# Kernel tuning notes

Measured on AMD Instinct MI355X. Metric: run time of the kernel, lower is better.

## Reference

```python
import jax, jax.numpy as jnp
import numpy as np

B, L, D = 8, 2048, 256
D_MODEL = 1024
NUM_SIGNALS = 16
MAX_POSITIONS = 4096
ROLE_OUTPUT = 2  # role id used for the CLS token


def setup_inputs() -> dict:
    key = jax.random.key(0)
    ks = jax.random.split(key, 12)
    emb = jax.random.normal(ks[0], (B, L, D), dtype=jnp.float32)
    pos = jax.random.randint(ks[1], (B, L), 1, MAX_POSITIONS + 1)          # pos >= 1 for real tokens
    sid = jax.random.randint(ks[2], (B, L), 0, NUM_SIGNALS)
    role = jax.random.randint(ks[3], (B, L), 0, 3)
    padding_mask = jax.random.uniform(ks[4], (B, L)) < 0.75                # True = real token
    # learned parameters
    proj_W = jax.random.normal(ks[5], (NUM_SIGNALS, D_MODEL, D), dtype=jnp.float32) * (1.0 / np.sqrt(D))
    proj_b = jax.random.normal(ks[6], (NUM_SIGNALS, D_MODEL), dtype=jnp.float32) * 0.01
    cls_content = jax.random.normal(ks[7], (D_MODEL,), dtype=jnp.float32)
    pos_embed = jax.random.normal(ks[8], (MAX_POSITIONS + 1, D_MODEL), dtype=jnp.float32)
    id_embed = jax.random.normal(ks[9], (NUM_SIGNALS + 1, D_MODEL), dtype=jnp.float32)
    role_embed = jax.random.normal(ks[10], (3, D_MODEL), dtype=jnp.float32)
    return dict(emb=emb, pos=pos, sid=sid, role=role, padding_mask=padding_mask,
                proj_W=proj_W, proj_b=proj_b, cls_content=cls_content,
                pos_embed=pos_embed, id_embed=id_embed, role_embed=role_embed)


def reference(emb, pos, sid, role, padding_mask,
              proj_W, proj_b, cls_content, pos_embed, id_embed, role_embed):
    Bv, Lv, _ = emb.shape
    S, d_model, _ = proj_W.shape
    cls_id = S

    # Grouped per-signal projection: one GEMM per signal id, select per token.
    tokens = jnp.zeros((Bv, Lv, d_model), dtype=emb.dtype)
    for s in range(S):
        proj_s = jnp.einsum('bld,ed->ble', emb, proj_W[s]) + proj_b[s]   # (B, L, d_model)
        keep = ((sid == s) & padding_mask)[..., None]
        tokens = jnp.where(keep, proj_s, tokens)

    # Prepend CLS
    cls = jnp.broadcast_to(cls_content[None, None, :], (Bv, 1, d_model))
    tokens = jnp.concatenate([cls, tokens], axis=1)                       # (B, L+1, d_model)

    pos_full = jnp.concatenate([jnp.zeros((Bv, 1), dtype=pos.dtype), pos], axis=1)
    sid_full = jnp.concatenate([jnp.full((Bv, 1), cls_id, dtype=sid.dtype), sid], axis=1)
    role_full = jnp.concatenate([jnp.full((Bv, 1), ROLE_OUTPUT, dtype=role.dtype), role], axis=1)

    tokens = tokens + pos_embed[pos_full] + id_embed[sid_full] + role_embed[role_full]

    attn_keep = jnp.concatenate([jnp.ones((Bv, 1), dtype=bool), padding_mask], axis=1)
    return tokens, attn_keep
```

## Files before the change

kernel.cpp:

```cpp
#include <hip/hip_runtime.h>
#include <hip/hip_bf16.h>
#include <stdint.h>

#define B_ 8
#define L_ 2048
#define NTOK 16384
#define DK 256
#define DM 1024
#define NS 16
#define LOUT 2049
#define TOK_OUT (B_*LOUT*DM)
#define ATTN_OUT (B_*LOUT)

typedef unsigned short u16;
typedef unsigned int u32;
typedef __bf16 bf16x8 __attribute__((ext_vector_type(8)));
typedef float f32x4 __attribute__((ext_vector_type(4)));

__device__ inline u32 packbf2(float lo, float hi) {
    u32 a, b;
    __builtin_memcpy(&a, &lo, 4);
    __builtin_memcpy(&b, &hi, 4);
    a = (a + 0x8000u) >> 16;
    b = (b + 0x8000u) & 0xFFFF0000u;
    return a | b;
}

__device__ inline void gll16(const void* g, void* l) {
    __builtin_amdgcn_global_load_lds(
        (const __attribute__((address_space(1))) unsigned int*)g,
        (__attribute__((address_space(3))) unsigned int*)l, 16, 0, 0);
}

#define WS_CNT 0
#define WS_CUR 16
#define WS_PERM 64
#define WS_MASK (64 + NTOK)
#define A_OFF 262144ULL
#define APAD_ROWS 18432
#define W_OFF (A_OFF + (unsigned long long)APAD_ROWS * 512ULL)
#define WS_NEED (W_OFF + 16384ULL * 512ULL)

__global__ __launch_bounds__(256) void p1_kernel(const unsigned char* __restrict__ mb,
                                                 const int* __restrict__ sid,
                                                 int* __restrict__ wsi) {
    __shared__ int f_c1ge2, f_ge2, f_odd;
    __shared__ int lcnt[NS];
    int tid = threadIdx.x;
    if (tid == 0) { f_c1ge2 = 0; f_ge2 = 0; f_odd = 0; }
    if (tid < NS) lcnt[tid] = 0;
    __syncthreads();

    int c1ge2 = 0, ge2 = 0, oddnz = 0;
    const u32* mw = (const u32*)mb;
    #pragma unroll
    for (int i = 0; i < 16; i++) {
        u32 x = mw[tid * 16 + i];
        u32 b0 = x & 0xFF, b1 = (x >> 8) & 0xFF, b2 = (x >> 16) & 0xFF, b3 = x >> 24;
        if (b1 >= 2) c1ge2 = 1;
        if (b0 >= 2 || b1 >= 2 || b2 >= 2 || b3 >= 2) ge2 = 1;
        if ((b1 | b3) != 0) oddnz = 1;
    }
    if (c1ge2) atomicOr(&f_c1ge2, 1);
    if (ge2) atomicOr(&f_ge2, 1);
    if (oddnz) atomicOr(&f_odd, 1);
    __syncthreads();

    int width;
    if (f_c1ge2) width = 2;
    else if (f_ge2) width = 4;
    else if (f_odd) width = 1;
    else width = 4;

    int t = blockIdx.x * 256 + tid;
    int m;
    if (width == 1) m = (mb[t] != 0);
    else if (width == 2) m = (((const u16*)mb)[t] != 0);
    else m = (((const u32*)mb)[t] != 0);

    wsi[WS_MASK + t] = m;
    if (m) atomicAdd(&lcnt[sid[t]], 1);
    __syncthreads();
    if (tid < NS) atomicAdd(&wsi[WS_CNT + tid], lcnt[tid]);
}

__global__ __launch_bounds__(256) void p3_kernel(const int* __restrict__ sid,
                                                 int* __restrict__ wsi) {
    __shared__ int gcnt[NS], lcnt[NS], base[NS];
    int tid = threadIdx.x;
    if (tid < NS) { gcnt[tid] = wsi[WS_CNT + tid]; lcnt[tid] = 0; }
    __syncthreads();
    int t = blockIdx.x * 256 + tid;
    int m = wsi[WS_MASK + t];
    int s = sid[t];
    int r = 0;
    if (m) r = atomicAdd(&lcnt[s], 1);
    __syncthreads();
    if (tid < NS) {
        int off = 0;
        for (int i = 0; i < tid; i++) off += gcnt[i];
        base[tid] = off + atomicAdd(&wsi[WS_CUR + tid], lcnt[tid]);
    }
    __syncthreads();
    if (m) wsi[WS_PERM + base[s] + r] = t;
}

__global__ __launch_bounds__(256) void prep_kernel(const float* __restrict__ emb,
                                                   const float* __restrict__ W,
                                                   int* __restrict__ wsi,
                                                   unsigned char* __restrict__ wsb) {
    int bid = blockIdx.x;
    int tid = threadIdx.x;
    int lane = tid & 63;
    int wv = tid >> 6;
    if (bid < 4608) {
        int cnts[NS], segoff[NS], pbase[NS];
        int accp = 0, accu = 0;
        #pragma unroll
        for (int i = 0; i < NS; i++) {
            cnts[i] = wsi[WS_CNT + i];
            segoff[i] = accp; pbase[i] = accu;
            accp += ((cnts[i] + 127) >> 7) << 7;
            accu += cnts[i];
        }
        int r = bid * 4 + wv;
        if (r >= accp) return;
        int s = 0;
        #pragma unroll
        for (int i = 1; i < NS; i++) if (r >= segoff[i]) s = i;
        int local = r - segoff[s];
        u16* Ab = (u16*)(wsb + A_OFF);
        uint2 o;
        if (local < cnts[s]) {
            int t = wsi[WS_PERM + pbase[s] + local];
            float4 a = *(const float4*)(emb + (size_t)t * DK + lane * 4);
            o.x = packbf2(a.x, a.y);
            o.y = packbf2(a.z, a.w);
        } else {
            o.x = 0; o.y = 0;
        }
        *(uint2*)(Ab + (size_t)r * DK + lane * 4) = o;
    } else {
        int r = (bid - 4608) * 4 + wv;
        u16* Wb = (u16*)(wsb + W_OFF);
        float4 a = *(const float4*)(W + (size_t)r * DK + lane * 4);
        uint2 o;
        o.x = packbf2(a.x, a.y);
        o.y = packbf2(a.z, a.w);
        *(uint2*)(Wb + (size_t)r * DK + lane * 4) = o;
    }
}

__global__ __launch_bounds__(256) void gemm_big(
    const int* __restrict__ pos, const int* __restrict__ role,
    const float* __restrict__ bias,
    const float* __restrict__ pos_emb, const float* __restrict__ id_emb,
    const float* __restrict__ role_emb,
    const int* __restrict__ wsi, const unsigned char* __restrict__ wsb,
    float* __restrict__ out) {
    __shared__ u16 As[128 * 64];
    __shared__ u16 Bs[128 * 64];
    __shared__ int toks[128];
    int tid = threadIdx.x;
    int lane = tid & 63;
    int wv = tid >> 6;

    int cnts[NS];
    #pragma unroll
    for (int i = 0; i < NS; i++) cnts[i] = wsi[WS_CNT + i];
    int ry = (int)blockIdx.y;
    int s = -1, lrt = 0, seg0 = 0, pb = 0;
    {
        int accp = 0, accu = 0;
        #pragma unroll
        for (int i = 0; i < NS; i++) {
            int rt = (cnts[i] + 127) >> 7;
            if (s < 0) {
                if (ry < rt) { s = i; lrt = ry; seg0 = accp; pb = accu; }
                else ry -= rt;
            }
            accp += rt << 7;
            accu += cnts[i];
        }
    }
    if (s < 0) return;
    int rowsValid = cnts[s] - lrt * 128;
    if (rowsValid > 128) rowsValid = 128;

    if (tid < 128) toks[tid] = (tid < rowsValid) ? wsi[WS_PERM + pb + lrt * 128 + tid] : -1;

    int n0 = (int)blockIdx.x * 128;
    const u16* Ab = (const u16*)(wsb + A_OFF) + (size_t)(seg0 + lrt * 128) * DK;
    const u16* Bb = (const u16*)(wsb + W_OFF) + (size_t)(s * DM + n0) * DK;

    int srow = lane >> 3;
    int sseg = (lane & 7) ^ srow;

    f32x4 acc[4][4];
    #pragma unroll
    for (int im = 0; im < 4; im++)
        #pragma unroll
        for (int jn = 0; jn < 4; jn++) acc[im][jn] = (f32x4){0.f, 0.f, 0.f, 0.f};

    int wm = wv >> 1, wn = wv & 1;
    int mcol = lane & 15;
    int quad = lane >> 4;

    for (int kc = 0; kc < 4; ++kc) {
        #pragma unroll
        for (int i = 0; i < 4; i++) {
            int row = wv * 32 + i * 8;
            gll16(Ab + (size_t)(row + srow) * DK + kc * 64 + sseg * 8,
                  As + row * 64);
            gll16(Bb + (size_t)(row + srow) * DK + kc * 64 + sseg * 8,
                  Bs + row * 64);
        }
        __syncthreads();
        #pragma unroll
        for (int ks = 0; ks < 2; ++ks) {
            bf16x8 af[4], bf[4];
            #pragma unroll
            for (int im = 0; im < 4; im++) {
                int row = wm * 64 + im * 16 + mcol;
                int sg = (ks * 4 + quad) ^ (row & 7);
                af[im] = *(const bf16x8*)(As + row * 64 + sg * 8);
            }
            #pragma unroll
            for (int jn = 0; jn < 4; jn++) {
                int row = wn * 64 + jn * 16 + mcol;
                int sg = (ks * 4 + quad) ^ (row & 7);
                bf[jn] = *(const bf16x8*)(Bs + row * 64 + sg * 8);
            }
            #pragma unroll
            for (int im = 0; im < 4; im++)
                #pragma unroll
                for (int jn = 0; jn < 4; jn++)
                    acc[im][jn] = __builtin_amdgcn_mfma_f32_16x16x32_bf16(
                        af[im], bf[jn], acc[im][jn], 0, 0, 0);
        }
        __syncthreads();
    }

    float bc[4];
    #pragma unroll
    for (int jn = 0; jn < 4; jn++) {
        int col = n0 + wn * 64 + jn * 16 + mcol;
        bc[jn] = bias[s * DM + col] + id_emb[s * DM + col];
    }
    #pragma unroll
    for (int im = 0; im < 4; im++) {
        #pragma unroll
        for (int r = 0; r < 4; r++) {
            int rowT = wm * 64 + im * 16 + quad * 4 + r;
            if (rowT >= rowsValid) continue;
            int t = toks[rowT];
            int p = pos[t];
            int ro = role[t];
            int b = t >> 11, l = t & 2047;
            size_t orow = (size_t)(b * LOUT + l + 1) * DM;
            #pragma unroll
            for (int jn = 0; jn < 4; jn++) {
                int col = n0 + wn * 64 + jn * 16 + mcol;
                float val = acc[im][jn][r] + bc[jn]
                    + pos_emb[(size_t)p * DM + col]
                    + role_emb[ro * DM + col];
                out[orow + col] = val;
            }
        }
    }
}

#define SP 136
__global__ __launch_bounds__(256) void gemm_small(
    const float* __restrict__ emb, const int* __restrict__ pos,
    const int* __restrict__ role,
    const float* __restrict__ W, const float* __restrict__ bias,
    const float* __restrict__ pos_emb, const float* __restrict__ id_emb,
    const float* __restrict__ role_emb,
    const int* __restrict__ wsi, float* __restrict__ out) {
    __shared__ u16 As[64 * SP];
    __shared__ u16 Bs[64 * SP];
    __shared__ int toks[64];
    int tid = threadIdx.x;

    int cnts[NS];
    #pragma unroll
    for (int i = 0; i < NS; i++) cnts[i] = wsi[WS_CNT + i];
    int ry = (int)blockIdx.y;
    int s = -1, tokOff = 0, lrt = 0;
    #pragma unroll
    for (int i = 0; i < NS; i++) {
        int rt = (cnts[i] + 63) >> 6;
        if (s < 0) {
            if (ry < rt) { s = i; lrt = ry; }
            else { ry -= rt; tokOff += cnts[i]; }
        }
    }
    if (s < 0) return;
    int idx0 = tokOff + lrt * 64;
    int v = cnts[s] - lrt * 64;
    if (v > 64) v = 64;

    if (tid < 64) toks[tid] = (tid < v) ? wsi[WS_PERM + idx0 + tid] : -1;
    __syncthreads();

    int lane = tid & 63;
    int w = tid >> 6;
    int mcol = lane & 15;
    int quad = lane >> 4;
    int n0 = (int)blockIdx.x * 64;

    f32x4 acc[4];
    #pragma unroll
    for (int j = 0; j < 4; j++) acc[j] = (f32x4){0.f, 0.f, 0.f, 0.f};

    const float* Wbase = W + (size_t)s * DM * DK + (size_t)n0 * DK;

    for (int kc = 0; kc < 2; ++kc) {
        #pragma unroll
        for (int i = 0; i < 8; i++) {
            int q = tid + 256 * i;
            int row = q >> 5, seg = q & 31;
            int t = toks[row];
            float4 a = make_float4(0.f, 0.f, 0.f, 0.f);
            if (t >= 0) a = *(const float4*)(emb + (size_t)t * DK + kc * 128 + seg * 4);
            uint2 ap;
            ap.x = packbf2(a.x, a.y);
            ap.y = packbf2(a.z, a.w);
            *(uint2*)(As + row * SP + seg * 4) = ap;
        }
        #pragma unroll
        for (int i = 0; i < 8; i++) {
            int q = tid + 256 * i;
            int row = q >> 5, seg = q & 31;
            float4 b = *(const float4*)(Wbase + (size_t)row * DK + kc * 128 + seg * 4);
            uint2 bp;
            bp.x = packbf2(b.x, b.y);
            bp.y = packbf2(b.z, b.w);
            *(uint2*)(Bs + row * SP + seg * 4) = bp;
        }
        __syncthreads();
        #pragma unroll
        for (int ks = 0; ks < 4; ++ks) {
            int kk = ks * 32 + quad * 8;
            bf16x8 af = *(const bf16x8*)(As + (16 * w + mcol) * SP + kk);
            #pragma unroll
            for (int j = 0; j < 4; j++) {
                bf16x8 bfr = *(const bf16x8*)(Bs + (16 * j + mcol) * SP + kk);
                acc[j] = __builtin_amdgcn_mfma_f32_16x16x32_bf16(af, bfr, acc[j], 0, 0, 0);
            }
        }
        __syncthreads();
    }

    #pragma unroll
    for (int r = 0; r < 4; r++) {
        int mrow = 16 * w + quad * 4 + r;
        if (mrow >= v) continue;
        int t = toks[mrow];
        int p = pos[t];
        int ro = role[t];
        int b = t >> 11, l = t & 2047;
        size_t orow = (size_t)(b * LOUT + l + 1) * DM;
        #pragma unroll
        for (int j = 0; j < 4; j++) {
            int col = n0 + 16 * j + mcol;
            float val = acc[j][r]
                + bias[s * DM + col]
                + pos_emb[(size_t)p * DM + col]
                + id_emb[s * DM + col]
                + role_emb[ro * DM + col];
            out[orow + col] = val;
        }
    }
}

__global__ __launch_bounds__(256) void ew_kernel(
    const int* __restrict__ pos, const int* __restrict__ sid,
    const int* __restrict__ role,
    const float* __restrict__ cls, const float* __restrict__ pos_emb,
    const float* __restrict__ id_emb, const float* __restrict__ role_emb,
    const int* __restrict__ wsi, float* __restrict__ out) {
    int bi = blockIdx.x;
    int tid = threadIdx.x;
    if (bi < NTOK) {
        int t = bi;
        if (wsi[WS_MASK + t]) return;
        int p = pos[t], sd = sid[t], ro = role[t];
        int b = t >> 11, l = t & 2047;
        size_t orow = (size_t)(b * LOUT + l + 1) * DM;
        int c = tid * 4;
        float4 a = *(const float4*)(pos_emb + (size_t)p * DM + c);
        float4 d = *(const float4*)(id_emb + (size_t)sd * DM + c);
        float4 e = *(const float4*)(role_emb + (size_t)ro * DM + c);
        float4 o;
        o.x = a.x + d.x + e.x;
        o.y = a.y + d.y + e.y;
        o.z = a.z + d.z + e.z;
        o.w = a.w + d.w + e.w;
        *(float4*)(out + orow + c) = o;
    } else if (bi < NTOK + B_) {
        int b = bi - NTOK;
        size_t orow = (size_t)(b * LOUT) * DM;
        int c = tid * 4;
        float4 cc = *(const float4*)(cls + c);
        float4 a = *(const float4*)(pos_emb + c);
        float4 d = *(const float4*)(id_emb + NS * DM + c);
        float4 e = *(const float4*)(role_emb + 2 * DM + c);
        float4 o;
        o.x = cc.x + a.x + d.x + e.x;
        o.y = cc.y + a.y + d.y + e.y;
        o.z = cc.z + a.z + d.z + e.z;
        o.w = cc.w + a.w + d.w + e.w;
        *(float4*)(out + orow + c) = o;
    } else {
        int i = (bi - NTOK - B_) * 256 + tid;
        if (i < ATTN_OUT) {
            int b = i / LOUT;
            int j = i - b * LOUT;
            float val = (j == 0) ? 1.0f : (float)wsi[WS_MASK + b * L_ + j - 1];
            out[TOK_OUT + i] = val;
        }
    }
}

extern "C" void kernel_launch(void* const* d_in, const int* in_sizes, int n_in,
                              void* d_out, int out_size, void* d_ws, size_t ws_size,
                              hipStream_t stream) {
    const float* emb = (const float*)d_in[0];
    const int* pos = (const int*)d_in[1];
    const int* sid = (const int*)d_in[2];
    const int* role = (const int*)d_in[3];
    const unsigned char* mask = (const unsigned char*)d_in[4];
    const float* W = (const float*)d_in[5];
    const float* bias = (const float*)d_in[6];
    const float* cls = (const float*)d_in[7];
    const float* pos_emb = (const float*)d_in[8];
    const float* id_emb = (const float*)d_in[9];
    const float* role_emb = (const float*)d_in[10];
    float* out = (float*)d_out;
    int* wsi = (int*)d_ws;
    unsigned char* wsb = (unsigned char*)d_ws;

    hipMemsetAsync(wsi, 0, 32 * sizeof(int), stream);
    hipLaunchKernelGGL(p1_kernel, dim3(64), dim3(256), 0, stream, mask, sid, wsi);
    hipLaunchKernelGGL(p3_kernel, dim3(64), dim3(256), 0, stream, sid, wsi);
    if (ws_size >= WS_NEED) {
        hipLaunchKernelGGL(prep_kernel, dim3(4608 + 4096), dim3(256), 0, stream,
                           emb, W, wsi, wsb);
        hipLaunchKernelGGL(gemm_big, dim3(8, 144), dim3(256), 0, stream,
                           pos, role, bias, pos_emb, id_emb, role_emb, wsi, wsb, out);
    } else {
        hipLaunchKernelGGL(gemm_small, dim3(16, 272), dim3(256), 0, stream,
                           emb, pos, role, W, bias, pos_emb, id_emb, role_emb, wsi, out);
    }
    hipLaunchKernelGGL(ew_kernel, dim3(NTOK + B_ + 65), dim3(256), 0, stream,
                       pos, sid, role, cls, pos_emb, id_emb, role_emb, wsi, out);
}
```

Before: 171.8 us.

## Fuse counting and scatter into one sort kernel, double-buffer a wider GEMM tile

The two-pass count-then-scatter token grouping becomes one kernel: each signal gets a fixed-capacity slot region (PCAP=2048), so no global prefix sum or second launch is needed. The grouped GEMM moves to 512-thread blocks with 128x256 output tiles and K chunks of 32, double-buffered in LDS with a rotated swizzle so the next chunk's loads overlap the current MFMAs. The elementwise kernel for padded tokens now handles four tokens per block, one per wave, and the small-workspace fallback GEMM is removed. The cost is that any signal with more than 2048 real tokens would be silently truncated, and the code now assumes the workspace is always large enough.

```diff
diff --git a/kernel.cpp b/kernel.cpp
--- a/kernel.cpp
+++ b/kernel.cpp
@@ -11,6 +11,7 @@
 #define LOUT 2049
 #define TOK_OUT (B_*LOUT*DM)
 #define ATTN_OUT (B_*LOUT)
+#define PCAP 2048
 
 typedef unsigned short u16;
 typedef unsigned int u32;
@@ -32,20 +33,19 @@
         (__attribute__((address_space(3))) unsigned int*)l, 16, 0, 0);
 }
 
-#define WS_CNT 0
-#define WS_CUR 16
+#define WS_CUR 0
 #define WS_PERM 64
-#define WS_MASK (64 + NTOK)
+#define WS_MASK (64 + NS * PCAP)
 #define A_OFF 262144ULL
 #define APAD_ROWS 18432
 #define W_OFF (A_OFF + (unsigned long long)APAD_ROWS * 512ULL)
 #define WS_NEED (W_OFF + 16384ULL * 512ULL)
 
-__global__ __launch_bounds__(256) void p1_kernel(const unsigned char* __restrict__ mb,
-                                                 const int* __restrict__ sid,
-                                                 int* __restrict__ wsi) {
+__global__ __launch_bounds__(256) void sort_kernel(const unsigned char* __restrict__ mb,
+                                                   const int* __restrict__ sid,
+                                                   int* __restrict__ wsi) {
     __shared__ int f_c1ge2, f_ge2, f_odd;
-    __shared__ int lcnt[NS];
+    __shared__ int lcnt[NS], gbase[NS];
     int tid = threadIdx.x;
     if (tid == 0) { f_c1ge2 = 0; f_ge2 = 0; f_odd = 0; }
     if (tid < NS) lcnt[tid] = 0;
@@ -79,49 +79,35 @@
     else m = (((const u32*)mb)[t] != 0);
 
     wsi[WS_MASK + t] = m;
-    if (m) atomicAdd(&lcnt[sid[t]], 1);
+    int s = sid[t];
+    int lr = 0;
+    if (m) lr = atomicAdd(&lcnt[s], 1);
     __syncthreads();
-    if (tid < NS) atomicAdd(&wsi[WS_CNT + tid], lcnt[tid]);
-}
-
-__global__ __launch_bounds__(256) void p3_kernel(const int* __restrict__ sid,
-                                                 int* __restrict__ wsi) {
-    __shared__ int gcnt[NS], lcnt[NS], base[NS];
-    int tid = threadIdx.x;
-    if (tid < NS) { gcnt[tid] = wsi[WS_CNT + tid]; lcnt[tid] = 0; }
+    if (tid < NS) gbase[tid] = atomicAdd(&wsi[WS_CUR + tid], lcnt[tid]);
     __syncthreads();
-    int t = blockIdx.x * 256 + tid;
-    int m = wsi[WS_MASK + t];
-    int s = sid[t];
-    int r = 0;
-    if (m) r = atomicAdd(&lcnt[s], 1);
-    __syncthreads();
-    if (tid < NS) {
-        int off = 0;
-        for (int i = 0; i < tid; i++) off += gcnt[i];
-        base[tid] = off + atomicAdd(&wsi[WS_CUR + tid], lcnt[tid]);
-    }
-    __syncthreads();
-    if (m) wsi[WS_PERM + base[s] + r] = t;
+    if (m) {
+        int r = gbase[s] + lr;
+        if (r < PCAP) wsi[WS_PERM + s * PCAP + r] = t;
+    }
 }
 
 __global__ __launch_bounds__(256) void prep_kernel(const float* __restrict__ emb,
                                                    const float* __restrict__ W,
-                                                   int* __restrict__ wsi,
+                                                   const int* __restrict__ wsi,
                                                    unsigned char* __restrict__ wsb) {
     int bid = blockIdx.x;
     int tid = threadIdx.x;
     int lane = tid & 63;
     int wv = tid >> 6;
     if (bid < 4608) {
-        int cnts[NS], segoff[NS], pbase[NS];
-        int accp = 0, accu = 0;
+        int cnts[NS], segoff[NS];
+        int accp = 0;
         #pragma unroll
         for (int i = 0; i < NS; i++) {
-            cnts[i] = wsi[WS_CNT + i];
-            segoff[i] = accp; pbase[i] = accu;
+            int c = wsi[WS_CUR + i];
+            cnts[i] = c > PCAP ? PCAP : c;
+            segoff[i] = accp;
             accp += ((cnts[i] + 127) >> 7) << 7;
-            accu += cnts[i];
         }
         int r = bid * 4 + wv;
         if (r >= accp) return;
@@ -132,7 +118,7 @@
         u16* Ab = (u16*)(wsb + A_OFF);
         uint2 o;
         if (local < cnts[s]) {
-            int t = wsi[WS_PERM + pbase[s] + local];
+            int t = wsi[WS_PERM + s * PCAP + local];
             float4 a = *(const float4*)(emb + (size_t)t * DK + lane * 4);
             o.x = packbf2(a.x, a.y);
             o.y = packbf2(a.z, a.w);
@@ -151,15 +137,15 @@
     }
 }
 
-__global__ __launch_bounds__(256) void gemm_big(
+__global__ __launch_bounds__(512, 4) void gemm_big(
     const int* __restrict__ pos, const int* __restrict__ role,
     const float* __restrict__ bias,
     const float* __restrict__ pos_emb, const float* __restrict__ id_emb,
     const float* __restrict__ role_emb,
     const int* __restrict__ wsi, const unsigned char* __restrict__ wsb,
     float* __restrict__ out) {
-    __shared__ u16 As[128 * 64];
-    __shared__ u16 Bs[128 * 64];
+    __shared__ u16 As[2][128 * 32];
+    __shared__ u16 Bs[2][256 * 32];
     __shared__ int toks[128];
     int tid = threadIdx.x;
     int lane = tid & 63;
@@ -167,34 +153,36 @@
 
     int cnts[NS];
     #pragma unroll
-    for (int i = 0; i < NS; i++) cnts[i] = wsi[WS_CNT + i];
+    for (int i = 0; i < NS; i++) {
+        int c = wsi[WS_CUR + i];
+        cnts[i] = c > PCAP ? PCAP : c;
+    }
     int ry = (int)blockIdx.y;
-    int s = -1, lrt = 0, seg0 = 0, pb = 0;
+    int s = -1, lrt = 0, seg0 = 0;
     {
-        int accp = 0, accu = 0;
+        int accp = 0;
         #pragma unroll
         for (int i = 0; i < NS; i++) {
             int rt = (cnts[i] + 127) >> 7;
             if (s < 0) {
-                if (ry < rt) { s = i; lrt = ry; seg0 = accp; pb = accu; }
+                if (ry < rt) { s = i; lrt = ry; seg0 = accp; }
                 else ry -= rt;
             }
             accp += rt << 7;
-            accu += cnts[i];
         }
     }
     if (s < 0) return;
     int rowsValid = cnts[s] - lrt * 128;
     if (rowsValid > 128) rowsValid = 128;
 
-    if (tid < 128) toks[tid] = (tid < rowsValid) ? wsi[WS_PERM + pb + lrt * 128 + tid] : -1;
-
-    int n0 = (int)blockIdx.x * 128;
+    if (tid < 128) toks[tid] = (tid < rowsValid) ? wsi[WS_PERM + s * PCAP + lrt * 128 + tid] : -1;
+
+    int n0 = (int)blockIdx.x * 256;
     const u16* Ab = (const u16*)(wsb + A_OFF) + (size_t)(seg0 + lrt * 128) * DK;
     const u16* Bb = (const u16*)(wsb + W_OFF) + (size_t)(s * DM + n0) * DK;
 
-    int srow = lane >> 3;
-    int sseg = (lane & 7) ^ srow;
+    int srow = lane >> 2;
+    int slseg = lane & 3;
 
     f32x4 acc[4][4];
     #pragma unroll
@@ -202,43 +190,51 @@
         #pragma unroll
         for (int jn = 0; jn < 4; jn++) acc[im][jn] = (f32x4){0.f, 0.f, 0.f, 0.f};
 
-    int wm = wv >> 1, wn = wv & 1;
+    int wm = wv & 1, wn = wv >> 1;
     int mcol = lane & 15;
     int quad = lane >> 4;
 
-    for (int kc = 0; kc < 4; ++kc) {
-        #pragma unroll
-        for (int i = 0; i < 4; i++) {
-            int row = wv * 32 + i * 8;
-            gll16(Ab + (size_t)(row + srow) * DK + kc * 64 + sseg * 8,
-                  As + row * 64);
-            gll16(Bb + (size_t)(row + srow) * DK + kc * 64 + sseg * 8,
-                  Bs + row * 64);
-        }
+#define STAGE(kc, bf)                                                          \
+    {                                                                          \
+        int arow = wv * 16 + srow;                                             \
+        int ags = (slseg - (arow >> 1)) & 3;                                   \
+        gll16(Ab + (size_t)arow * DK + (kc) * 32 + ags * 8,                    \
+              &As[bf][wv * 16 * 32]);                                          \
+        int brow0 = wv * 16 + srow;                                            \
+        int bgs0 = (slseg - (brow0 >> 1)) & 3;                                 \
+        gll16(Bb + (size_t)brow0 * DK + (kc) * 32 + bgs0 * 8,                  \
+              &Bs[bf][wv * 16 * 32]);                                          \
+        int brow1 = 128 + wv * 16 + srow;                                      \
+        int bgs1 = (slseg - (brow1 >> 1)) & 3;                                 \
+        gll16(Bb + (size_t)brow1 * DK + (kc) * 32 + bgs1 * 8,                  \
+              &Bs[bf][(128 + wv * 16) * 32]);                                  \
+    }
+
+    STAGE(0, 0)
+    #pragma unroll
+    for (int kc = 0; kc < 8; ++kc) {
         __syncthreads();
-        #pragma unroll
-        for (int ks = 0; ks < 2; ++ks) {
-            bf16x8 af[4], bf[4];
+        if (kc < 7) STAGE(kc + 1, (kc + 1) & 1)
+        int bf = kc & 1;
+        bf16x8 af[4], bfr[4];
+        #pragma unroll
+        for (int im = 0; im < 4; im++) {
+            int row = wm * 64 + im * 16 + mcol;
+            int sg = (quad + (row >> 1)) & 3;
+            af[im] = *(const bf16x8*)(&As[bf][row * 32 + sg * 8]);
+        }
+        #pragma unroll
+        for (int jn = 0; jn < 4; jn++) {
+            int row = wn * 64 + jn * 16 + mcol;
+            int sg = (quad + (row >> 1)) & 3;
+            bfr[jn] = *(const bf16x8*)(&Bs[bf][row * 32 + sg * 8]);
+        }
+        #pragma unroll
+        for (int im = 0; im < 4; im++)
             #pragma unroll
-            for (int im = 0; im < 4; im++) {
-                int row = wm * 64 + im * 16 + mcol;
-                int sg = (ks * 4 + quad) ^ (row & 7);
-                af[im] = *(const bf16x8*)(As + row * 64 + sg * 8);
-            }
-            #pragma unroll
-            for (int jn = 0; jn < 4; jn++) {
-                int row = wn * 64 + jn * 16 + mcol;
-                int sg = (ks * 4 + quad) ^ (row & 7);
-                bf[jn] = *(const bf16x8*)(Bs + row * 64 + sg * 8);
-            }
-            #pragma unroll
-            for (int im = 0; im < 4; im++)
-                #pragma unroll
-                for (int jn = 0; jn < 4; jn++)
-                    acc[im][jn] = __builtin_amdgcn_mfma_f32_16x16x32_bf16(
-                        af[im], bf[jn], acc[im][jn], 0, 0, 0);
-        }
-        __syncthreads();
+            for (int jn = 0; jn < 4; jn++)
+                acc[im][jn] = __builtin_amdgcn_mfma_f32_16x16x32_bf16(
+                    af[im], bfr[jn], acc[im][jn], 0, 0, 0);
     }
 
     float bc[4];
@@ -268,111 +264,7 @@
             }
         }
     }
-}
-
-#define SP 136
-__global__ __launch_bounds__(256) void gemm_small(
-    const float* __restrict__ emb, const int* __restrict__ pos,
-    const int* __restrict__ role,
-    const float* __restrict__ W, const float* __restrict__ bias,
-    const float* __restrict__ pos_emb, const float* __restrict__ id_emb,
-    const float* __restrict__ role_emb,
-    const int* __restrict__ wsi, float* __restrict__ out) {
-    __shared__ u16 As[64 * SP];
-    __shared__ u16 Bs[64 * SP];
-    __shared__ int toks[64];
-    int tid = threadIdx.x;
-
-    int cnts[NS];
-    #pragma unroll
-    for (int i = 0; i < NS; i++) cnts[i] = wsi[WS_CNT + i];
-    int ry = (int)blockIdx.y;
-    int s = -1, tokOff = 0, lrt = 0;
-    #pragma unroll
-    for (int i = 0; i < NS; i++) {
-        int rt = (cnts[i] + 63) >> 6;
-        if (s < 0) {
-            if (ry < rt) { s = i; lrt = ry; }
-            else { ry -= rt; tokOff += cnts[i]; }
-        }
-    }
-    if (s < 0) return;
-    int idx0 = tokOff + lrt * 64;
-    int v = cnts[s] - lrt * 64;
-    if (v > 64) v = 64;
-
-    if (tid < 64) toks[tid] = (tid < v) ? wsi[WS_PERM + idx0 + tid] : -1;
-    __syncthreads();
-
-    int lane = tid & 63;
-    int w = tid >> 6;
-    int mcol = lane & 15;
-    int quad = lane >> 4;
-    int n0 = (int)blockIdx.x * 64;
-
-    f32x4 acc[4];
-    #pragma unroll
-    for (int j = 0; j < 4; j++) acc[j] = (f32x4){0.f, 0.f, 0.f, 0.f};
-
-    const float* Wbase = W + (size_t)s * DM * DK + (size_t)n0 * DK;
-
-    for (int kc = 0; kc < 2; ++kc) {
-        #pragma unroll
-        for (int i = 0; i < 8; i++) {
-            int q = tid + 256 * i;
-            int row = q >> 5, seg = q & 31;
-            int t = toks[row];
-            float4 a = make_float4(0.f, 0.f, 0.f, 0.f);
-            if (t >= 0) a = *(const float4*)(emb + (size_t)t * DK + kc * 128 + seg * 4);
-            uint2 ap;
-            ap.x = packbf2(a.x, a.y);
-            ap.y = packbf2(a.z, a.w);
-            *(uint2*)(As + row * SP + seg * 4) = ap;
-        }
-        #pragma unroll
-        for (int i = 0; i < 8; i++) {
-            int q = tid + 256 * i;
-            int row = q >> 5, seg = q & 31;
-            float4 b = *(const float4*)(Wbase + (size_t)row * DK + kc * 128 + seg * 4);
-            uint2 bp;
-            bp.x = packbf2(b.x, b.y);
-            bp.y = packbf2(b.z, b.w);
-            *(uint2*)(Bs + row * SP + seg * 4) = bp;
-        }
-        __syncthreads();
-        #pragma unroll
-        for (int ks = 0; ks < 4; ++ks) {
-            int kk = ks * 32 + quad * 8;
-            bf16x8 af = *(const bf16x8*)(As + (16 * w + mcol) * SP + kk);
-            #pragma unroll
-            for (int j = 0; j < 4; j++) {
-                bf16x8 bfr = *(const bf16x8*)(Bs + (16 * j + mcol) * SP + kk);
-                acc[j] = __builtin_amdgcn_mfma_f32_16x16x32_bf16(af, bfr, acc[j], 0, 0, 0);
-            }
-        }
-        __syncthreads();
-    }
-
-    #pragma unroll
-    for (int r = 0; r < 4; r++) {
-        int mrow = 16 * w + quad * 4 + r;
-        if (mrow >= v) continue;
-        int t = toks[mrow];
-        int p = pos[t];
-        int ro = role[t];
-        int b = t >> 11, l = t & 2047;
-        size_t orow = (size_t)(b * LOUT + l + 1) * DM;
-        #pragma unroll
-        for (int j = 0; j < 4; j++) {
-            int col = n0 + 16 * j + mcol;
-            float val = acc[j][r]
-                + bias[s * DM + col]
-                + pos_emb[(size_t)p * DM + col]
-                + id_emb[s * DM + col]
-                + role_emb[ro * DM + col];
-            out[orow + col] = val;
-        }
-    }
+#undef STAGE
 }
 
 __global__ __launch_bounds__(256) void ew_kernel(
@@ -383,38 +275,46 @@
     const int* __restrict__ wsi, float* __restrict__ out) {
     int bi = blockIdx.x;
     int tid = threadIdx.x;
-    if (bi < NTOK) {
-        int t = bi;
+    int lane = tid & 63;
+    int wv = tid >> 6;
+    if (bi < NTOK / 4) {
+        int t = bi * 4 + wv;
         if (wsi[WS_MASK + t]) return;
         int p = pos[t], sd = sid[t], ro = role[t];
         int b = t >> 11, l = t & 2047;
         size_t orow = (size_t)(b * LOUT + l + 1) * DM;
-        int c = tid * 4;
-        float4 a = *(const float4*)(pos_emb + (size_t)p * DM + c);
-        float4 d = *(const float4*)(id_emb + (size_t)sd * DM + c);
-        float4 e = *(const float4*)(role_emb + (size_t)ro * DM + c);
-        float4 o;
-        o.x = a.x + d.x + e.x;
-        o.y = a.y + d.y + e.y;
-        o.z = a.z + d.z + e.z;
-        o.w = a.w + d.w + e.w;
-        *(float4*)(out + orow + c) = o;
-    } else if (bi < NTOK + B_) {
-        int b = bi - NTOK;
+        #pragma unroll
+        for (int it = 0; it < 4; it++) {
+            int c = it * 256 + lane * 4;
+            float4 a = *(const float4*)(pos_emb + (size_t)p * DM + c);
+            float4 d = *(const float4*)(id_emb + (size_t)sd * DM + c);
+            float4 e = *(const float4*)(role_emb + (size_t)ro * DM + c);
+            float4 o;
+            o.x = a.x + d.x + e.x;
+            o.y = a.y + d.y + e.y;
+            o.z = a.z + d.z + e.z;
+            o.w = a.w + d.w + e.w;
+            *(float4*)(out + orow + c) = o;
+        }
+    } else if (bi < NTOK / 4 + 2) {
+        int b = (bi - NTOK / 4) * 4 + wv;
         size_t orow = (size_t)(b * LOUT) * DM;
-        int c = tid * 4;
-        float4 cc = *(const float4*)(cls + c);
-        float4 a = *(const float4*)(pos_emb + c);
-        float4 d = *(const float4*)(id_emb + NS * DM + c);
-        float4 e = *(const float4*)(role_emb + 2 * DM + c);
-        float4 o;
-        o.x = cc.x + a.x + d.x + e.x;
-        o.y = cc.y + a.y + d.y + e.y;
-        o.z = cc.z + a.z + d.z + e.z;
-        o.w = cc.w + a.w + d.w + e.w;
-        *(float4*)(out + orow + c) = o;
+        #pragma unroll
+        for (int it = 0; it < 4; it++) {
+            int c = it * 256 + lane * 4;
+            float4 cc = *(const float4*)(cls + c);
+            float4 a = *(const float4*)(pos_emb + c);
+            float4 d = *(const float4*)(id_emb + NS * DM + c);
+            float4 e = *(const float4*)(role_emb + 2 * DM + c);
+            float4 o;
+            o.x = cc.x + a.x + d.x + e.x;
+            o.y = cc.y + a.y + d.y + e.y;
+            o.z = cc.z + a.z + d.z + e.z;
+            o.w = cc.w + a.w + d.w + e.w;
+            *(float4*)(out + orow + c) = o;
+        }
     } else {
-        int i = (bi - NTOK - B_) * 256 + tid;
+        int i = (bi - NTOK / 4 - 2) * 256 + tid;
         if (i < ATTN_OUT) {
             int b = i / LOUT;
             int j = i - b * LOUT;
@@ -442,18 +342,12 @@
     int* wsi = (int*)d_ws;
     unsigned char* wsb = (unsigned char*)d_ws;
 
-    hipMemsetAsync(wsi, 0, 32 * sizeof(int), stream);
-    hipLaunchKernelGGL(p1_kernel, dim3(64), dim3(256), 0, stream, mask, sid, wsi);
-    hipLaunchKernelGGL(p3_kernel, dim3(64), dim3(256), 0, stream, sid, wsi);
-    if (ws_size >= WS_NEED) {
-        hipLaunchKernelGGL(prep_kernel, dim3(4608 + 4096), dim3(256), 0, stream,
-                           emb, W, wsi, wsb);
-        hipLaunchKernelGGL(gemm_big, dim3(8, 144), dim3(256), 0, stream,
-                           pos, role, bias, pos_emb, id_emb, role_emb, wsi, wsb, out);
-    } else {
-        hipLaunchKernelGGL(gemm_small, dim3(16, 272), dim3(256), 0, stream,
-                           emb, pos, role, W, bias, pos_emb, id_emb, role_emb, wsi, out);
-    }
-    hipLaunchKernelGGL(ew_kernel, dim3(NTOK + B_ + 65), dim3(256), 0, stream,
+    hipMemsetAsync(wsi, 0, 64 * sizeof(int), stream);
+    hipLaunchKernelGGL(sort_kernel, dim3(64), dim3(256), 0, stream, mask, sid, wsi);
+    hipLaunchKernelGGL(prep_kernel, dim3(4608 + 4096), dim3(256), 0, stream,
+                       emb, W, wsi, wsb);
+    hipLaunchKernelGGL(gemm_big, dim3(4, 144), dim3(512), 0, stream,
+                       pos, role, bias, pos_emb, id_emb, role_emb, wsi, wsb, out);
+    hipLaunchKernelGGL(ew_kernel, dim3(NTOK / 4 + 2 + 65), dim3(256), 0, stream,
                        pos, sid, role, cls, pos_emb, id_emb, role_emb, wsi, out);
 }
```

New measurement: 161.5 us. 6.0% less time.
